# Optimization experiments

Hardware: AMD Instinct MI355X
Metric: run time of the kernel (lower is better)

The kernel has to match this reference:

```python
import jax, jax.numpy as jnp
import numpy as np

# Instant-NGP hash grid constants (match init_kwargs)
N_MAX, N_MIN = 2048.0, 16.0
L, T, F, DIM = 16, 2**19, 2, 3
NV = 2**DIM  # 8 corners of a voxel
# primes stored as int32 in the original (2654435761 wraps negative) -> replicate exactly
PIS = jnp.asarray(np.array([1, 2654435761, 805459861], dtype=np.uint32).astype(np.int32))
# bin_mask[v, d] = True -> corner v takes floor along dim d
_neigs = np.arange(NV, dtype=np.int64)[:, None]
_dims = np.arange(DIM, dtype=np.int64)[None, :]
BIN_MASK = jnp.asarray((_neigs & (1 << _dims)) == 0)  # [8, 3]
# per-level grid resolutions N_l = N_min * b**l
_b = np.exp((np.log(N_MAX) - np.log(N_MIN)) / L)
SCALES = jnp.asarray((N_MIN * _b ** np.arange(L)).astype(np.float32))  # [L]


def setup_inputs() -> dict:
    key = jax.random.key(0)
    k1, k2 = jax.random.split(key)
    N = 2_000_000
    x = jax.random.uniform(k1, (N, DIM), dtype=jnp.float32)  # points in [0,1)^3 (mu=0, sigma=1)
    # per-level embedding tables, init U(-1e-4, 1e-4) as in the torch module
    W = jax.random.uniform(k2, (L, T, F), minval=-1e-4, maxval=1e-4, dtype=jnp.float32)
    return {"x": x, "W": W}


def _hash(idxs):
    # idxs: [N, 8, 3] int32. int32 wraparound multiply matches low 32 bits of the
    # torch int64 product; since T is a power of two and Python-style mod of a
    # negative by a positive only depends on the low log2(T) bits, result matches.
    prod = idxs * PIS  # [N, 8, 3] int32 (wraps)
    h = prod[..., 0] ^ prod[..., 1] ^ prod[..., 2]
    return h % T  # jnp remainder follows sign of divisor -> nonnegative


def _encode(x, W):
    def level(carry, level_args):
        scale, Wl = level_args
        un_x = x * scale                                   # [N, 3]
        x0 = un_x.astype(jnp.int32)                        # trunc == floor for x >= 0
        diff = jax.lax.stop_gradient(un_x - x0.astype(un_x.dtype))  # [N, 3], detached as in torch
        # corner integer coords: floor where bin_mask else floor+1
        idxs = jnp.where(BIN_MASK[None], x0[:, None, :], x0[:, None, :] + 1)  # [N, 8, 3]
        fv = Wl[_hash(idxs)]                               # [N, 8, F] gather
        wts = jnp.where(BIN_MASK[None], 1.0 - diff[:, None, :], diff[:, None, :])
        wts = wts.prod(axis=-1, keepdims=True)             # [N, 8, 1] trilinear weights
        return carry, (fv * wts).sum(axis=-2)              # [N, F]

    _, ys = jax.lax.scan(level, 0, (SCALES, W))            # [L, N, F]
    # original writes level l into y[:, l*F:(l+1)*F]
    return jnp.transpose(ys, (1, 0, 2)).reshape(x.shape[0], L * F)


def reference(x, W):
    return _encode(x, W)
```

## Files before the change

### kernel.cpp

```cpp
#include <hip/hip_runtime.h>
#include <hip/hip_fp16.h>
#include <math.h>

#define NLEV 16
#define TBLN (1u << 19)
#define TMASK (TBLN - 1u)
#define NPT 4
#define NPTL 16
#define NPTL2 8
#define PR1 2654435761u
#define PR2 805459861u

typedef float f32x4 __attribute__((ext_vector_type(4)));
typedef unsigned int u32;
typedef unsigned int u32x2 __attribute__((ext_vector_type(2)));
typedef unsigned int u32x4 __attribute__((ext_vector_type(4)));

struct ScaleArgs { float s[NLEV]; };

#define DU0 18
#define DU1 23
#define DU2 31
#define GU0 0
#define GU1 5832
#define GU2 17999
#define GUTOT 47790
#define DD2 31
#define DD3 41
#define DD4 55
#define DD5 75
#define GO2 0
#define GO3 28830
#define GO4 96070
#define GO5 259420
#define GPTOT 675670

static __device__ __forceinline__ u32 packf2(float a, float b) {
    __half2 h = __floats2half2_rn(a, b);
    return __builtin_bit_cast(u32, h);
}
static __device__ __forceinline__ float2 unpack16(u32 u) {
    __half2 h = __builtin_bit_cast(__half2, u);
    return __half22float2(h);
}

__global__ __launch_bounds__(256)
void convert_w(const float* __restrict__ W, u32* __restrict__ Wh, int np4)
{
    int i = blockIdx.x * blockDim.x + threadIdx.x;
    if (i >= np4) return;
    const f32x4* src = reinterpret_cast<const f32x4*>(W) + (size_t)i * 2;
    f32x4 A = __builtin_nontemporal_load(src);
    f32x4 B = __builtin_nontemporal_load(src + 1);
    u32x4 o = { packf2(A.x, A.y), packf2(A.z, A.w),
                packf2(B.x, B.y), packf2(B.z, B.w) };
    __builtin_nontemporal_store(o, reinterpret_cast<u32x4*>(Wh) + i);
}

__global__ __launch_bounds__(256)
void build_unpaired(const float* __restrict__ Wlf, u32* __restrict__ Gu, int D, int P)
{
    int v = blockIdx.x * blockDim.x + threadIdx.x;
    if (v >= P) return;
    int ix = v % D;
    int rest = v / D;
    int iy = rest % D;
    int iz = rest / D;
    u32 h = (((u32)iy * PR1) ^ ((u32)iz * PR2) ^ (u32)ix) & TMASK;
    float2 f = *reinterpret_cast<const float2*>(Wlf + (size_t)h * 2u);
    Gu[v] = packf2(f.x, f.y);
}

__global__ __launch_bounds__(256)
void build_dense(const float* __restrict__ Wlf, u32x2* __restrict__ Gpl, int D, int P)
{
    int v = blockIdx.x * blockDim.x + threadIdx.x;
    if (v >= P) return;
    int Dx = D - 1;
    int ix = v % Dx;
    int rest = v / Dx;
    int iy = rest % D;
    int iz = rest / D;
    u32 e = ((u32)iy * PR1) ^ ((u32)iz * PR2);
    u32 h0 = (e ^ (u32)ix) & TMASK;
    u32 h1 = (e ^ (u32)(ix + 1)) & TMASK;
    float2 f0 = *reinterpret_cast<const float2*>(Wlf + (size_t)h0 * 2u);
    float2 f1 = *reinterpret_cast<const float2*>(Wlf + (size_t)h1 * 2u);
    u32x2 o = { packf2(f0.x, f0.y), packf2(f1.x, f1.y) };
    Gpl[v] = o;
}

template<int D>
static __device__ __forceinline__ u32 lds_interp(const u32* g, float ux, float uy, float uz)
{
    int ix = (int)ux, iy = (int)uy, iz = (int)uz;
    float dx = ux - (float)ix, dy = uy - (float)iy, dz = uz - (float)iz;
    int b = (iz * D + iy) * D + ix;
    u32 c0 = g[b],             c1 = g[b + 1];
    u32 c2 = g[b + D],         c3 = g[b + D + 1];
    u32 c4 = g[b + D * D],     c5 = g[b + D * D + 1];
    u32 c6 = g[b + D * D + D], c7 = g[b + D * D + D + 1];
    float wxl = 1.f - dx, wxh = dx;
    float wyl = 1.f - dy, wyh = dy;
    float wzl = 1.f - dz, wzh = dz;
    float ax = 0.f, ay = 0.f;
    float2 f;
    f = unpack16(c0); { float w = (wxl * wyl) * wzl; ax = fmaf(f.x, w, ax); ay = fmaf(f.y, w, ay); }
    f = unpack16(c1); { float w = (wxh * wyl) * wzl; ax = fmaf(f.x, w, ax); ay = fmaf(f.y, w, ay); }
    f = unpack16(c2); { float w = (wxl * wyh) * wzl; ax = fmaf(f.x, w, ax); ay = fmaf(f.y, w, ay); }
    f = unpack16(c3); { float w = (wxh * wyh) * wzl; ax = fmaf(f.x, w, ax); ay = fmaf(f.y, w, ay); }
    f = unpack16(c4); { float w = (wxl * wyl) * wzh; ax = fmaf(f.x, w, ax); ay = fmaf(f.y, w, ay); }
    f = unpack16(c5); { float w = (wxh * wyl) * wzh; ax = fmaf(f.x, w, ax); ay = fmaf(f.y, w, ay); }
    f = unpack16(c6); { float w = (wxl * wyh) * wzh; ax = fmaf(f.x, w, ax); ay = fmaf(f.y, w, ay); }
    f = unpack16(c7); { float w = (wxh * wyh) * wzh; ax = fmaf(f.x, w, ax); ay = fmaf(f.y, w, ay); }
    return packf2(ax, ay);
}

template<int D>
__global__ __launch_bounds__(256)
void lds_level(const float* __restrict__ x, const u32* __restrict__ Gu,
               u32* __restrict__ scl, float scale, int N)
{
    __shared__ u32 g[D * D * D];
    for (int i = threadIdx.x; i < D * D * D; i += 256) g[i] = Gu[i];
    __syncthreads();

    int base = blockIdx.x * (256 * NPTL);
    #pragma unroll 4
    for (int i = 0; i < NPTL; ++i) {
        int n = base + i * 256 + (int)threadIdx.x;
        if (n < N) {
            float px = __builtin_nontemporal_load(&x[(size_t)n * 3 + 0]);
            float py = __builtin_nontemporal_load(&x[(size_t)n * 3 + 1]);
            float pz = __builtin_nontemporal_load(&x[(size_t)n * 3 + 2]);
            __builtin_nontemporal_store(
                lds_interp<D>(g, px * scale, py * scale, pz * scale), scl + n);
        }
    }
}

template<int D>
__global__ __launch_bounds__(512)
void lds_level_dyn(const float* __restrict__ x, const u32* __restrict__ Gu,
                   u32* __restrict__ scl, float scale, int N)
{
    extern __shared__ u32 g[];
    for (int i = threadIdx.x; i < D * D * D; i += 512) g[i] = Gu[i];
    __syncthreads();

    int base = blockIdx.x * (512 * NPTL2);
    #pragma unroll 4
    for (int i = 0; i < NPTL2; ++i) {
        int n = base + i * 512 + (int)threadIdx.x;
        if (n < N) {
            float px = __builtin_nontemporal_load(&x[(size_t)n * 3 + 0]);
            float py = __builtin_nontemporal_load(&x[(size_t)n * 3 + 1]);
            float pz = __builtin_nontemporal_load(&x[(size_t)n * 3 + 2]);
            __builtin_nontemporal_store(
                lds_interp<D>(g, px * scale, py * scale, pz * scale), scl + n);
        }
    }
}


template<int D>
static __device__ __forceinline__ void dense_body(
    const float* __restrict__ x, const u32x2* __restrict__ Gp,
    u32* __restrict__ scl, float scale, int N, int TOT, int t)
{
    constexpr int Dx = D - 1;
    constexpr int zstep = D * Dx;

    int nn[NPT];
    float dx[NPT], dy[NPT], dz[NPT];
    int base[NPT];
    u32x2 P0[NPT], P1[NPT], P2[NPT], P3[NPT];

    #pragma unroll
    for (int i = 0; i < NPT; ++i) {
        int n = t + i * TOT;
        if (n > N - 1) n = N - 1;
        nn[i] = n;
        float px = __builtin_nontemporal_load(&x[(size_t)n * 3 + 0]);
        float py = __builtin_nontemporal_load(&x[(size_t)n * 3 + 1]);
        float pz = __builtin_nontemporal_load(&x[(size_t)n * 3 + 2]);
        float ux = px * scale, uy = py * scale, uz = pz * scale;
        int ix = (int)ux, iy = (int)uy, iz = (int)uz;
        dx[i] = ux - (float)ix;
        dy[i] = uy - (float)iy;
        dz[i] = uz - (float)iz;
        base[i] = (iz * D + iy) * Dx + ix;
    }

    #pragma unroll
    for (int i = 0; i < NPT; ++i) {
        int b = base[i];
        P0[i] = Gp[b];
        P1[i] = Gp[b + Dx];
        P2[i] = Gp[b + zstep];
        P3[i] = Gp[b + zstep + Dx];
    }

    #pragma unroll
    for (int i = 0; i < NPT; ++i) {
        float ax = 0.f, ay = 0.f;
        float wxl = 1.f - dx[i], wxh = dx[i];
        float wyl = 1.f - dy[i], wyh = dy[i];
        float wzl = 1.f - dz[i], wzh = dz[i];
        {
            float2 f0 = unpack16(P0[i].x), f1 = unpack16(P0[i].y);
            float w0 = (wxl * wyl) * wzl, w1 = (wxh * wyl) * wzl;
            ax = fmaf(f0.x, w0, ax); ay = fmaf(f0.y, w0, ay);
            ax = fmaf(f1.x, w1, ax); ay = fmaf(f1.y, w1, ay);
        }
        {
            float2 f0 = unpack16(P1[i].x), f1 = unpack16(P1[i].y);
            float w0 = (wxl * wyh) * wzl, w1 = (wxh * wyh) * wzl;
            ax = fmaf(f0.x, w0, ax); ay = fmaf(f0.y, w0, ay);
            ax = fmaf(f1.x, w1, ax); ay = fmaf(f1.y, w1, ay);
        }
        {
            float2 f0 = unpack16(P2[i].x), f1 = unpack16(P2[i].y);
            float w0 = (wxl * wyl) * wzh, w1 = (wxh * wyl) * wzh;
            ax = fmaf(f0.x, w0, ax); ay = fmaf(f0.y, w0, ay);
            ax = fmaf(f1.x, w1, ax); ay = fmaf(f1.y, w1, ay);
        }
        {
            float2 f0 = unpack16(P3[i].x), f1 = unpack16(P3[i].y);
            float w0 = (wxl * wyh) * wzh, w1 = (wxh * wyh) * wzh;
            ax = fmaf(f0.x, w0, ax); ay = fmaf(f0.y, w0, ay);
            ax = fmaf(f1.x, w1, ax); ay = fmaf(f1.y, w1, ay);
        }
        __builtin_nontemporal_store(packf2(ax, ay), scl + nn[i]);
    }
}

static __device__ __forceinline__ void hash_body(
    const float* __restrict__ x, const u32* __restrict__ Wl,
    u32* __restrict__ scl, float scale, int N, int TOT, int t)
{
    int nn[NPT];
    float dx[NPT], dy[NPT], dz[NPT];
    u32 a0[NPT], a1[NPT], a2[NPT];
    u32 fv[NPT][8];

    #pragma unroll
    for (int i = 0; i < NPT; ++i) {
        int n = t + i * TOT;
        if (n > N - 1) n = N - 1;
        nn[i] = n;
        float px = __builtin_nontemporal_load(&x[(size_t)n * 3 + 0]);
        float py = __builtin_nontemporal_load(&x[(size_t)n * 3 + 1]);
        float pz = __builtin_nontemporal_load(&x[(size_t)n * 3 + 2]);
        float ux = px * scale, uy = py * scale, uz = pz * scale;
        int ix = (int)ux, iy = (int)uy, iz = (int)uz;
        dx[i] = ux - (float)ix;
        dy[i] = uy - (float)iy;
        dz[i] = uz - (float)iz;
        a0[i] = (unsigned)ix;
        a1[i] = (unsigned)iy * PR1;
        a2[i] = (unsigned)iz * PR2;
    }

    #pragma unroll
    for (int i = 0; i < NPT; ++i) {
        u32 b0 = a0[i] + 1u, b1 = a1[i] + PR1, b2 = a2[i] + PR2;
        u32 E[4] = { a1[i] ^ a2[i], b1 ^ a2[i], a1[i] ^ b2, b1 ^ b2 };
        if ((a0[i] & 1u) == 0u) {
            #pragma unroll
            for (int j = 0; j < 4; ++j) {
                u32 hl = (E[j] ^ a0[i]) & TMASK;
                u32x2 p = *reinterpret_cast<const u32x2*>(Wl + (hl & ~1u));
                u32 lo = (hl & 1u) ? p.y : p.x;
                u32 hi = (hl & 1u) ? p.x : p.y;
                fv[i][2 * j + 0] = lo;
                fv[i][2 * j + 1] = hi;
            }
        } else {
            #pragma unroll
            for (int j = 0; j < 4; ++j) {
                u32 hl = (E[j] ^ a0[i]) & TMASK;
                u32 hh = (E[j] ^ b0) & TMASK;
                fv[i][2 * j + 0] = Wl[hl];
                fv[i][2 * j + 1] = Wl[hh];
            }
        }
    }

    #pragma unroll
    for (int i = 0; i < NPT; ++i) {
        float ax = 0.f, ay = 0.f;
        #pragma unroll
        for (int v = 0; v < 8; ++v) {
            float wx = (v & 1) ? dx[i] : 1.f - dx[i];
            float wy = (v & 2) ? dy[i] : 1.f - dy[i];
            float wz = (v & 4) ? dz[i] : 1.f - dz[i];
            float w = (wx * wy) * wz;
            float2 f = unpack16(fv[i][v]);
            ax = fmaf(f.x, w, ax);
            ay = fmaf(f.y, w, ay);
        }
        __builtin_nontemporal_store(packf2(ax, ay), scl + nn[i]);
    }
}

__global__ __launch_bounds__(256)
void fused_levels(const float* __restrict__ x, const u32* __restrict__ Wh,
                  const u32x2* __restrict__ Gp, u32* __restrict__ scratch,
                  ScaleArgs sc, int N, int TOT, int BPL, int lstart)
{
    int li = blockIdx.x / BPL;
    int lvl = li + lstart;
    int t = (blockIdx.x - li * BPL) * blockDim.x + threadIdx.x;
    if (t >= TOT) return;
    float scale = sc.s[lvl];
    u32* scl = scratch + (size_t)lvl * (size_t)N;

    switch (lvl) {
        case 2: dense_body<DD2>(x, Gp + GO2, scl, scale, N, TOT, t); break;
        case 3: dense_body<DD3>(x, Gp + GO3, scl, scale, N, TOT, t); break;
        case 4: dense_body<DD4>(x, Gp + GO4, scl, scale, N, TOT, t); break;
        case 5: dense_body<DD5>(x, Gp + GO5, scl, scale, N, TOT, t); break;
        default:
            hash_body(x, Wh + (size_t)(lvl - 6) * TBLN, scl, scale, N, TOT, t);
            break;
    }
}

__global__ __launch_bounds__(256)
void transpose_kernel(const u32* __restrict__ sc, float* __restrict__ out, int N)
{
    __shared__ u32 lds[16][257];
    int P0 = blockIdx.x * 256;
    int t = threadIdx.x;
    #pragma unroll
    for (int l = 0; l < NLEV; ++l) {
        int n = P0 + t;
        if (n < N) lds[l][t] = __builtin_nontemporal_load(sc + (size_t)l * N + n);
    }
    __syncthreads();
    int w = t >> 6, l6 = t & 63;
    #pragma unroll
    for (int k = 0; k < 8; ++k) {
        int p = w * 64 + k * 8 + (l6 >> 3);
        int c = l6 & 7;
        if (P0 + p < N) {
            float2 f0 = unpack16(lds[2 * c][p]);
            float2 f1 = unpack16(lds[2 * c + 1][p]);
            f32x4 v = { f0.x, f0.y, f1.x, f1.y };
            __builtin_nontemporal_store(v,
                reinterpret_cast<f32x4*>(out + (size_t)(P0 + p) * 32u + (size_t)c * 4u));
        }
    }
}

__global__ __launch_bounds__(256)
void hashenc_fallback(const float* __restrict__ x, const float* __restrict__ W,
                      float* __restrict__ out, ScaleArgs sc, int N)
{
    int n = blockIdx.x * blockDim.x + threadIdx.x;
    if (n >= N) return;
    float px = x[(size_t)n * 3 + 0];
    float py = x[(size_t)n * 3 + 1];
    float pz = x[(size_t)n * 3 + 2];
    float acc[2 * NLEV];
    #pragma unroll
    for (int l = 0; l < NLEV; ++l) {
        float s = sc.s[l];
        float ux = px * s, uy = py * s, uz = pz * s;
        int ix = (int)ux, iy = (int)uy, iz = (int)uz;
        float dx = ux - (float)ix, dy = uy - (float)iy, dz = uz - (float)iz;
        unsigned a0 = (unsigned)ix;
        unsigned a1 = (unsigned)iy * PR1;
        unsigned a2 = (unsigned)iz * PR2;
        unsigned b0 = a0 + 1u, b1 = a1 + PR1, b2 = a2 + PR2;
        const float* Wl = W + (size_t)l * TBLN * 2u;
        float ax = 0.f, ay = 0.f;
        #pragma unroll
        for (int v = 0; v < 8; ++v) {
            unsigned h = ((v & 1) ? b0 : a0) ^ ((v & 2) ? b1 : a1) ^ ((v & 4) ? b2 : a2);
            h &= TMASK;
            float wx = (v & 1) ? dx : 1.f - dx;
            float wy = (v & 2) ? dy : 1.f - dy;
            float wz = (v & 4) ? dz : 1.f - dz;
            float w = (wx * wy) * wz;
            const float2 fvv = *reinterpret_cast<const float2*>(Wl + (size_t)h * 2u);
            ax = fmaf(fvv.x, w, ax);
            ay = fmaf(fvv.y, w, ay);
        }
        acc[2 * l + 0] = ax;
        acc[2 * l + 1] = ay;
    }
    float4* o = reinterpret_cast<float4*>(out + (size_t)n * (2 * NLEV));
    #pragma unroll
    for (int j = 0; j < 8; ++j)
        o[j] = make_float4(acc[4 * j + 0], acc[4 * j + 1], acc[4 * j + 2], acc[4 * j + 3]);
}

extern "C" void kernel_launch(void* const* d_in, const int* in_sizes, int n_in,
                              void* d_out, int out_size, void* d_ws, size_t ws_size,
                              hipStream_t stream) {
    const float* x = (const float*)d_in[0];
    const float* W = (const float*)d_in[1];
    float* out = (float*)d_out;
    int N = in_sizes[0] / 3;

    ScaleArgs sc;
    double b = exp((log(2048.0) - log(16.0)) / 16.0);
    for (int l = 0; l < NLEV; ++l) {
        double p;
        switch (l) {
            case 0: p = 1.0; break;
            case 1: p = b;   break;
            case 2: p = b * b; break;
            default: p = pow(b, (double)l); break;
        }
        sc.s[l] = (float)(16.0 * p);
    }

    size_t wh_u32 = (size_t)(NLEV - 6) * TBLN;
    size_t gp_u32 = (size_t)GPTOT * 2u;
    size_t gu_u32 = (size_t)GUTOT;
    size_t scr_u32 = (size_t)NLEV * (size_t)N;
    size_t need = (wh_u32 + gp_u32 + gu_u32 + scr_u32) * sizeof(u32);

    if (ws_size >= need) {
        u32* Wh = (u32*)d_ws;
        u32x2* Gp = reinterpret_cast<u32x2*>(Wh + wh_u32);
        u32* Gu = Wh + wh_u32 + gp_u32;
        u32* scratch = Gu + gu_u32;

        size_t l2_lds_bytes = (size_t)DU2 * DU2 * DU2 * sizeof(u32);
        bool lvl2_lds = (hipFuncSetAttribute(
                             (const void*)&lds_level_dyn<DU2>,
                             hipFuncAttributeMaxDynamicSharedMemorySize,
                             (int)l2_lds_bytes) == hipSuccess);

        int np4 = (int)(wh_u32 / 4);
        hipLaunchKernelGGL(convert_w, dim3((np4 + 255) / 256), dim3(256), 0, stream,
                           W + (size_t)6 * TBLN * 2u, Wh, np4);

        {
            int P0c = DU0 * DU0 * DU0;
            hipLaunchKernelGGL(build_unpaired, dim3((P0c + 255) / 256), dim3(256), 0, stream,
                               W + 0, Gu + GU0, DU0, P0c);
            int P1c = DU1 * DU1 * DU1;
            hipLaunchKernelGGL(build_unpaired, dim3((P1c + 255) / 256), dim3(256), 0, stream,
                               W + (size_t)1 * TBLN * 2u, Gu + GU1, DU1, P1c);
            int P2c = DU2 * DU2 * DU2;
            hipLaunchKernelGGL(build_unpaired, dim3((P2c + 255) / 256), dim3(256), 0, stream,
                               W + (size_t)2 * TBLN * 2u, Gu + GU2, DU2, P2c);
        }

        const int Dl[4] = { DD2, DD3, DD4, DD5 };
        const int Ol[4] = { GO2, GO3, GO4, GO5 };
        for (int i = 0; i < 4; ++i) {
            int l = 2 + i;
            int P = (Dl[i] - 1) * Dl[i] * Dl[i];
            hipLaunchKernelGGL(build_dense, dim3((P + 255) / 256), dim3(256), 0, stream,
                               W + (size_t)l * TBLN * 2u, Gp + Ol[i], Dl[i], P);
        }

        {
            int blocks = (N + 256 * NPTL - 1) / (256 * NPTL);
            hipLaunchKernelGGL(lds_level<DU0>, dim3(blocks), dim3(256), 0, stream,
                               x, Gu + GU0, scratch + 0, sc.s[0], N);
            hipLaunchKernelGGL(lds_level<DU1>, dim3(blocks), dim3(256), 0, stream,
                               x, Gu + GU1, scratch + (size_t)N, sc.s[1], N);
        }

        if (lvl2_lds) {
            int blocks = (N + 512 * NPTL2 - 1) / (512 * NPTL2);
            hipLaunchKernelGGL(lds_level_dyn<DU2>, dim3(blocks), dim3(512),
                               l2_lds_bytes, stream,
                               x, Gu + GU2, scratch + (size_t)2 * N, sc.s[2], N);
        }

        int lstart = lvl2_lds ? 3 : 2;
        int TOT = (N + NPT - 1) / NPT;
        int BPL = (TOT + 255) / 256;
        hipLaunchKernelGGL(fused_levels, dim3((16 - lstart) * BPL), dim3(256), 0, stream,
                           x, Wh, Gp, scratch, sc, N, TOT, BPL, lstart);

        int gt = (N + 255) / 256;
        hipLaunchKernelGGL(transpose_kernel, dim3(gt), dim3(256), 0, stream,
                           scratch, out, N);
    } else {
        int grid = (N + 255) / 256;
        hipLaunchKernelGGL(hashenc_fallback, dim3(grid), dim3(256), 0, stream,
                           x, W, out, sc, N);
    }
}
```

Measured before the change: 627.3 us.

## Pack 2x2 corner quads for levels 3-4 and add 4-aligned hash fetch path

Levels 3 and 4 now use a precomputed grid where each cell stores all four x/y corners as one 16-byte record, so each point needs two vector loads instead of four paired loads. The hash levels gain a branch for x-index parity 1 mod 4 that reads an aligned 16-byte group and selects both x-neighbours from it, replacing two scalar gathers. The cost is larger prebuilt tables (more build traffic and cache footprint) and extra select logic with more divergent branches.

```diff
diff --git a/kernel.cpp b/kernel.cpp
--- a/kernel.cpp
+++ b/kernel.cpp
@@ -26,14 +26,15 @@
 #define GU2 17999
 #define GUTOT 47790
 #define DD2 31
+#define DD5 75
+#define PO2 0
+#define PO5 28830
+#define GPTOT2 445080
 #define DD3 41
 #define DD4 55
-#define DD5 75
-#define GO2 0
-#define GO3 28830
-#define GO4 96070
-#define GO5 259420
-#define GPTOT 675670
+#define QO3 0
+#define QO4 65600
+#define GQTOT 225980
 
 static __device__ __forceinline__ u32 packf2(float a, float b) {
     __half2 h = __floats2half2_rn(a, b);
@@ -42,6 +43,11 @@
 static __device__ __forceinline__ float2 unpack16(u32 u) {
     __half2 h = __builtin_bit_cast(__half2, u);
     return __half22float2(h);
+}
+static __device__ __forceinline__ u32 sel4(u32x4 P, u32 idx) {
+    u32 s0 = (idx & 1u) ? P.y : P.x;
+    u32 s1 = (idx & 1u) ? P.w : P.z;
+    return (idx & 2u) ? s1 : s0;
 }
 
 __global__ __launch_bounds__(256)
@@ -88,6 +94,31 @@
     float2 f1 = *reinterpret_cast<const float2*>(Wlf + (size_t)h1 * 2u);
     u32x2 o = { packf2(f0.x, f0.y), packf2(f1.x, f1.y) };
     Gpl[v] = o;
+}
+
+__global__ __launch_bounds__(256)
+void build_dense16(const float* __restrict__ Wlf, u32x4* __restrict__ Gql, int D, int P)
+{
+    int v = blockIdx.x * blockDim.x + threadIdx.x;
+    if (v >= P) return;
+    int Dx = D - 1;
+    int ix = v % Dx;
+    int rest = v / Dx;
+    int iy = rest % Dx;
+    int iz = rest / Dx;
+    u32 ey0 = ((u32)iy * PR1) ^ ((u32)iz * PR2);
+    u32 ey1 = ((u32)(iy + 1) * PR1) ^ ((u32)iz * PR2);
+    u32 h00 = (ey0 ^ (u32)ix) & TMASK;
+    u32 h10 = (ey0 ^ (u32)(ix + 1)) & TMASK;
+    u32 h01 = (ey1 ^ (u32)ix) & TMASK;
+    u32 h11 = (ey1 ^ (u32)(ix + 1)) & TMASK;
+    float2 f00 = *reinterpret_cast<const float2*>(Wlf + (size_t)h00 * 2u);
+    float2 f10 = *reinterpret_cast<const float2*>(Wlf + (size_t)h10 * 2u);
+    float2 f01 = *reinterpret_cast<const float2*>(Wlf + (size_t)h01 * 2u);
+    float2 f11 = *reinterpret_cast<const float2*>(Wlf + (size_t)h11 * 2u);
+    u32x4 o = { packf2(f00.x, f00.y), packf2(f10.x, f10.y),
+                packf2(f01.x, f01.y), packf2(f11.x, f11.y) };
+    Gql[v] = o;
 }
 
 template<int D>
@@ -235,6 +266,60 @@
     }
 }
 
+template<int D>
+static __device__ __forceinline__ void dense16_body(
+    const float* __restrict__ x, const u32x4* __restrict__ Gq,
+    u32* __restrict__ scl, float scale, int N, int TOT, int t)
+{
+    constexpr int Dx = D - 1;
+    constexpr int zstep = Dx * Dx;
+
+    int nn[NPT];
+    float dx[NPT], dy[NPT], dz[NPT];
+    int base[NPT];
+    u32x4 Q0[NPT], Q1[NPT];
+
+    #pragma unroll
+    for (int i = 0; i < NPT; ++i) {
+        int n = t + i * TOT;
+        if (n > N - 1) n = N - 1;
+        nn[i] = n;
+        float px = __builtin_nontemporal_load(&x[(size_t)n * 3 + 0]);
+        float py = __builtin_nontemporal_load(&x[(size_t)n * 3 + 1]);
+        float pz = __builtin_nontemporal_load(&x[(size_t)n * 3 + 2]);
+        float ux = px * scale, uy = py * scale, uz = pz * scale;
+        int ix = (int)ux, iy = (int)uy, iz = (int)uz;
+        dx[i] = ux - (float)ix;
+        dy[i] = uy - (float)iy;
+        dz[i] = uz - (float)iz;
+        base[i] = (iz * Dx + iy) * Dx + ix;
+    }
+
+    #pragma unroll
+    for (int i = 0; i < NPT; ++i) {
+        Q0[i] = Gq[base[i]];
+        Q1[i] = Gq[base[i] + zstep];
+    }
+
+    #pragma unroll
+    for (int i = 0; i < NPT; ++i) {
+        float ax = 0.f, ay = 0.f;
+        float wxl = 1.f - dx[i], wxh = dx[i];
+        float wyl = 1.f - dy[i], wyh = dy[i];
+        float wzl = 1.f - dz[i], wzh = dz[i];
+        float2 f;
+        f = unpack16(Q0[i].x); { float w = (wxl * wyl) * wzl; ax = fmaf(f.x, w, ax); ay = fmaf(f.y, w, ay); }
+        f = unpack16(Q0[i].y); { float w = (wxh * wyl) * wzl; ax = fmaf(f.x, w, ax); ay = fmaf(f.y, w, ay); }
+        f = unpack16(Q0[i].z); { float w = (wxl * wyh) * wzl; ax = fmaf(f.x, w, ax); ay = fmaf(f.y, w, ay); }
+        f = unpack16(Q0[i].w); { float w = (wxh * wyh) * wzl; ax = fmaf(f.x, w, ax); ay = fmaf(f.y, w, ay); }
+        f = unpack16(Q1[i].x); { float w = (wxl * wyl) * wzh; ax = fmaf(f.x, w, ax); ay = fmaf(f.y, w, ay); }
+        f = unpack16(Q1[i].y); { float w = (wxh * wyl) * wzh; ax = fmaf(f.x, w, ax); ay = fmaf(f.y, w, ay); }
+        f = unpack16(Q1[i].z); { float w = (wxl * wyh) * wzh; ax = fmaf(f.x, w, ax); ay = fmaf(f.y, w, ay); }
+        f = unpack16(Q1[i].w); { float w = (wxh * wyh) * wzh; ax = fmaf(f.x, w, ax); ay = fmaf(f.y, w, ay); }
+        __builtin_nontemporal_store(packf2(ax, ay), scl + nn[i]);
+    }
+}
+
 static __device__ __forceinline__ void hash_body(
     const float* __restrict__ x, const u32* __restrict__ Wl,
     u32* __restrict__ scl, float scale, int N, int TOT, int t)
@@ -266,15 +351,23 @@
     for (int i = 0; i < NPT; ++i) {
         u32 b0 = a0[i] + 1u, b1 = a1[i] + PR1, b2 = a2[i] + PR2;
         u32 E[4] = { a1[i] ^ a2[i], b1 ^ a2[i], a1[i] ^ b2, b1 ^ b2 };
-        if ((a0[i] & 1u) == 0u) {
+        u32 par = a0[i] & 3u;
+        if ((par & 1u) == 0u) {
             #pragma unroll
             for (int j = 0; j < 4; ++j) {
                 u32 hl = (E[j] ^ a0[i]) & TMASK;
                 u32x2 p = *reinterpret_cast<const u32x2*>(Wl + (hl & ~1u));
-                u32 lo = (hl & 1u) ? p.y : p.x;
-                u32 hi = (hl & 1u) ? p.x : p.y;
-                fv[i][2 * j + 0] = lo;
-                fv[i][2 * j + 1] = hi;
+                fv[i][2 * j + 0] = (hl & 1u) ? p.y : p.x;
+                fv[i][2 * j + 1] = (hl & 1u) ? p.x : p.y;
+            }
+        } else if (par == 1u) {
+            #pragma unroll
+            for (int j = 0; j < 4; ++j) {
+                u32 hl = (E[j] ^ a0[i]) & TMASK;
+                u32x4 P = *reinterpret_cast<const u32x4*>(Wl + (hl & ~3u));
+                u32 il = hl & 3u;
+                fv[i][2 * j + 0] = sel4(P, il);
+                fv[i][2 * j + 1] = sel4(P, il ^ 3u);
             }
         } else {
             #pragma unroll
@@ -306,7 +399,8 @@
 
 __global__ __launch_bounds__(256)
 void fused_levels(const float* __restrict__ x, const u32* __restrict__ Wh,
-                  const u32x2* __restrict__ Gp, u32* __restrict__ scratch,
+                  const u32x2* __restrict__ Gp, const u32x4* __restrict__ Gq,
+                  u32* __restrict__ scratch,
                   ScaleArgs sc, int N, int TOT, int BPL, int lstart)
 {
     int li = blockIdx.x / BPL;
@@ -317,10 +411,10 @@
     u32* scl = scratch + (size_t)lvl * (size_t)N;
 
     switch (lvl) {
-        case 2: dense_body<DD2>(x, Gp + GO2, scl, scale, N, TOT, t); break;
-        case 3: dense_body<DD3>(x, Gp + GO3, scl, scale, N, TOT, t); break;
-        case 4: dense_body<DD4>(x, Gp + GO4, scl, scale, N, TOT, t); break;
-        case 5: dense_body<DD5>(x, Gp + GO5, scl, scale, N, TOT, t); break;
+        case 2: dense_body<DD2>(x, Gp + PO2, scl, scale, N, TOT, t); break;
+        case 3: dense16_body<DD3>(x, Gq + QO3, scl, scale, N, TOT, t); break;
+        case 4: dense16_body<DD4>(x, Gq + QO4, scl, scale, N, TOT, t); break;
+        case 5: dense_body<DD5>(x, Gp + PO5, scl, scale, N, TOT, t); break;
         default:
             hash_body(x, Wh + (size_t)(lvl - 6) * TBLN, scl, scale, N, TOT, t);
             break;
@@ -419,15 +513,17 @@
     }
 
     size_t wh_u32 = (size_t)(NLEV - 6) * TBLN;
-    size_t gp_u32 = (size_t)GPTOT * 2u;
+    size_t gp_u32 = (size_t)GPTOT2 * 2u;
+    size_t gq_u32 = (size_t)GQTOT * 4u;
     size_t gu_u32 = (size_t)GUTOT;
     size_t scr_u32 = (size_t)NLEV * (size_t)N;
-    size_t need = (wh_u32 + gp_u32 + gu_u32 + scr_u32) * sizeof(u32);
+    size_t need = (wh_u32 + gp_u32 + gq_u32 + gu_u32 + scr_u32) * sizeof(u32);
 
     if (ws_size >= need) {
         u32* Wh = (u32*)d_ws;
         u32x2* Gp = reinterpret_cast<u32x2*>(Wh + wh_u32);
-        u32* Gu = Wh + wh_u32 + gp_u32;
+        u32x4* Gq = reinterpret_cast<u32x4*>(Wh + wh_u32 + gp_u32);
+        u32* Gu = Wh + wh_u32 + gp_u32 + gq_u32;
         u32* scratch = Gu + gu_u32;
 
         size_t l2_lds_bytes = (size_t)DU2 * DU2 * DU2 * sizeof(u32);
@@ -452,13 +548,22 @@
                                W + (size_t)2 * TBLN * 2u, Gu + GU2, DU2, P2c);
         }
 
-        const int Dl[4] = { DD2, DD3, DD4, DD5 };
-        const int Ol[4] = { GO2, GO3, GO4, GO5 };
-        for (int i = 0; i < 4; ++i) {
-            int l = 2 + i;
-            int P = (Dl[i] - 1) * Dl[i] * Dl[i];
-            hipLaunchKernelGGL(build_dense, dim3((P + 255) / 256), dim3(256), 0, stream,
-                               W + (size_t)l * TBLN * 2u, Gp + Ol[i], Dl[i], P);
+        {
+            int P2 = (DD2 - 1) * DD2 * DD2;
+            hipLaunchKernelGGL(build_dense, dim3((P2 + 255) / 256), dim3(256), 0, stream,
+                               W + (size_t)2 * TBLN * 2u, Gp + PO2, DD2, P2);
+            int P5 = (DD5 - 1) * DD5 * DD5;
+            hipLaunchKernelGGL(build_dense, dim3((P5 + 255) / 256), dim3(256), 0, stream,
+                               W + (size_t)5 * TBLN * 2u, Gp + PO5, DD5, P5);
+        }
+
+        {
+            int P3 = DD3 * (DD3 - 1) * (DD3 - 1);
+            hipLaunchKernelGGL(build_dense16, dim3((P3 + 255) / 256), dim3(256), 0, stream,
+                               W + (size_t)3 * TBLN * 2u, Gq + QO3, DD3, P3);
+            int P4 = DD4 * (DD4 - 1) * (DD4 - 1);
+            hipLaunchKernelGGL(build_dense16, dim3((P4 + 255) / 256), dim3(256), 0, stream,
+                               W + (size_t)4 * TBLN * 2u, Gq + QO4, DD4, P4);
         }
 
         {
@@ -480,7 +585,7 @@
         int TOT = (N + NPT - 1) / NPT;
         int BPL = (TOT + 255) / 256;
         hipLaunchKernelGGL(fused_levels, dim3((16 - lstart) * BPL), dim3(256), 0, stream,
-                           x, Wh, Gp, scratch, sc, N, TOT, BPL, lstart);
+                           x, Wh, Gp, Gq, scratch, sc, N, TOT, BPL, lstart);
 
         int gt = (N + 255) / 256;
         hipLaunchKernelGGL(transpose_kernel, dim3(gt), dim3(256), 0, stream,
```

Measured after the change: 607.0 us. 1.03x faster.
